# Optimization experiments

Measured on AMD Instinct MI355X. Metric: run time of the kernel, lower is better.

Reference implementation:

```python
import jax, jax.numpy as jnp
import numpy as np

BSZ, L, DIM = 2, 255, 128


def setup_inputs() -> dict:
    key = jax.random.key(0)
    k = jax.random.split(key, 8)
    d = DIM
    inv = 1.0 / np.sqrt(d)
    return {
        "x": jax.random.normal(k[0], (BSZ, L, L, d), jnp.float32),
        "mask": jax.random.randint(k[1], (BSZ, L, L), 0, 2, dtype=jnp.int32),
        "pos_embed_w": jax.random.normal(k[2], (2, d), jnp.float32) * 0.1,
        "h_qkv_w": jax.random.normal(k[3], (3 * d, d), jnp.float32) * inv,
        "h_qkv_b": jnp.zeros((3 * d,), jnp.float32),
        "v_qkv_w": jax.random.normal(k[4], (3 * d, d), jnp.float32) * inv,
        "v_qkv_b": jnp.zeros((3 * d,), jnp.float32),
        "dense_w": jax.random.normal(k[5], (d, 2 * d), jnp.float32) * (1.0 / np.sqrt(2 * d)),
        "dense_b": jnp.zeros((d,), jnp.float32),
        "ln1_g": jnp.ones((d,), jnp.float32),
        "ln1_b": jnp.zeros((d,), jnp.float32),
        "conv1_w": jax.random.normal(k[6], (d, d, 3, 3), jnp.float32) * (1.0 / np.sqrt(9 * d)),
        "conv2_w": jax.random.normal(k[7], (d, d, 3, 3), jnp.float32) * (1.0 / np.sqrt(9 * d)),
        "ln2_g": jnp.ones((d,), jnp.float32),
        "ln2_b": jnp.zeros((d,), jnp.float32),
    }


def _layer_norm(t, g, b, eps=1e-5):
    mu = t.mean(-1, keepdims=True)
    var = ((t - mu) ** 2).mean(-1, keepdims=True)
    return (t - mu) / jnp.sqrt(var + eps) * g + b


def _forward(x, mask, pos_embed_w, h_qkv_w, h_qkv_b, v_qkv_w, v_qkv_b,
             dense_w, dense_b, ln1_g, ln1_b, conv1_w, conv2_w, ln2_g, ln2_b):
    # dropout is identity (eval mode)
    bsz, L_, w, d = x.shape
    scale = np.sqrt(d)
    x = jnp.clip(x, -1000.0, 1000.0)

    # RoFormer sinusoidal table for w positions: sin/cos each (w, d//2)
    freq = 1.0 / (10000.0 ** (np.arange(0, d, 2, dtype=np.float64) / d))
    ang = np.arange(w, dtype=np.float64)[:, None] * freq[None, :]
    sin = jnp.asarray(np.sin(ang), x.dtype)
    cos = jnp.asarray(np.cos(ang), x.dtype)

    # triangular position bias: columns < w//2 get embed[0], rest embed[1]
    pos_idx = jnp.concatenate([
        jnp.zeros((w // 2,), jnp.int32), jnp.ones((w - w // 2,), jnp.int32)])
    x = x + pos_embed_w[pos_idx][None, None]  # (bsz, L, w, d)

    maskf = mask.reshape(-1, w).astype(x.dtype)            # (R, w), 1 = masked
    row_valid = mask.reshape(-1, w).sum(-1) != w            # (R,)
    add_mask = maskf[:, None, :] * -10000.0                 # (R, 1, w)

    def rotary(t):
        x1, x2 = t[..., 0::2], t[..., 1::2]
        r1 = x1 * cos - x2 * sin
        r2 = x2 * cos + x1 * sin
        return jnp.stack([r1, r2], axis=-1).reshape(t.shape)

    def attn_branch(scores, Wqkv, bqkv):
        # scores: (R, w, d)
        qkv = jnp.clip(scores @ Wqkv.T + bqkv, -10000.0, 10000.0)
        q, k, v = jnp.split(qkv, 3, axis=-1)
        q, k = rotary(q), rotary(k)
        a = jnp.clip(jnp.einsum('rqd,rkd->rqk', q, k) / scale, -10000.0, 10000.0)
        a = jax.nn.softmax(a + add_mask, axis=-1)
        a = jnp.where(maskf[:, None, :] > 0, 0.0, a)  # masked_fill after softmax
        return a @ v

    h_v = attn_branch(x.reshape(-1, w, d), h_qkv_w, h_qkv_b)

    # roll columns by (col - w//2) along rows, then flip columns
    # flipped[b,n,c] = x[b, (n - (w-1-c) + w//2) % L, w-1-c]
    cc = (w - 1) - jnp.arange(w)                                  # (w,)
    row_idx = (jnp.arange(L_)[:, None] - cc[None, :] + w // 2) % L_  # (L, w)
    v_scores = x[:, row_idx, cc[None, :]]                          # (bsz, L, w, d)
    v_v = attn_branch(v_scores.reshape(-1, w, d), v_qkv_w, v_qkv_b)

    v = jnp.concatenate([h_v, v_v], axis=-1) @ dense_w.T + dense_b
    # rows that are fully masked were never written in the torch scatter -> zero
    v = jnp.where(row_valid[:, None, None], v, 0.0)
    v = _layer_norm(v + x.reshape(-1, w, d), ln1_g, ln1_b)

    v4 = v.reshape(bsz, L_, w, d).transpose(0, 3, 1, 2)  # NCHW
    mb = mask[:, None, :, :] > 0                          # (bsz, 1, L, w)

    def mconv(t, kern):
        t = jnp.where(mb, 0.0, t)
        return jax.lax.conv_general_dilated(
            t, kern, (1, 1), 'SAME',
            dimension_numbers=('NCHW', 'OIHW', 'NCHW'))

    c = mconv(v4, conv1_w)
    c = jax.nn.gelu(c, approximate=False)
    c = mconv(c, conv2_w)
    c = c.transpose(0, 2, 3, 1).reshape(-1, w, d)
    out = _layer_norm(c + v, ln2_g, ln2_b)
    return out.reshape(bsz, L_, w, d)


def reference(x, mask, pos_embed_w, h_qkv_w, h_qkv_b, v_qkv_w, v_qkv_b,
              dense_w, dense_b, ln1_g, ln1_b, conv1_w, conv2_w, ln2_g, ln2_b):
    return _forward(x, mask, pos_embed_w, h_qkv_w, h_qkv_b, v_qkv_w, v_qkv_b,
                    dense_w, dense_b, ln1_g, ln1_b, conv1_w, conv2_w, ln2_g, ln2_b)
```

## Files before the change

### kernel.cpp

```cpp
#include <hip/hip_runtime.h>
#include <hip/hip_bf16.h>
#include <math.h>

constexpr int BSZ = 2;
constexpr int LL  = 255;
constexpr int WW  = 255;
constexpr int DD  = 128;
constexpr int RR  = BSZ * LL;
constexpr int GG  = RR * WW;

typedef __attribute__((ext_vector_type(8))) short bf16x8;
typedef __attribute__((ext_vector_type(4))) float f32x4;
typedef unsigned short ushort_t;

__device__ __forceinline__ float clip1k(float v){ return fminf(fmaxf(v, -1000.f), 1000.f); }
__device__ __forceinline__ float clipT(float v){ return fminf(fmaxf(v, -10000.f), 10000.f); }
__device__ __forceinline__ unsigned short f2bf(float f){
    unsigned int u = __float_as_uint(f);
    unsigned int r = u + 0x7fffu + ((u >> 16) & 1u);
    return (unsigned short)(r >> 16);
}
__device__ __forceinline__ float bf2f(ushort_t h){
    return __uint_as_float(((unsigned)h) << 16);
}

__global__ __launch_bounds__(64) void k_tables(const int* __restrict__ mask,
                                               float* __restrict__ sintab,
                                               float* __restrict__ costab,
                                               float* __restrict__ rv)
{
    int bid = blockIdx.x, lane = threadIdx.x;
    if (bid < RR) {
        const int* mr = mask + bid * WW;
        int s = 0;
        for (int j = lane; j < WW; j += 64) s += mr[j];
        #pragma unroll
        for (int off = 32; off > 0; off >>= 1) s += __shfl_xor(s, off);
        if (lane == 0) rv[bid] = (s != WW) ? 1.f : 0.f;
    } else {
        int base = (bid - RR) * 256;
        for (int k = 0; k < 4; k++) {
            int idx = base + k * 64 + lane;
            if (idx < WW * 64) {
                int p = idx >> 6, t = idx & 63;
                double freq = exp((double)t * (-9.210340371976184 / 64.0));
                double a = (double)p * freq;
                sintab[idx] = (float)sin(a);
                costab[idx] = (float)cos(a);
            }
        }
    }
}

__global__ __launch_bounds__(256) void k_wconv(const float* __restrict__ w1,
                                               const float* __restrict__ w2,
                                               ushort_t* __restrict__ Wt1,
                                               ushort_t* __restrict__ Wt2)
{
    int idx = blockIdx.x * 256 + threadIdx.x;
    if (idx >= 2 * 147456) return;
    int buf = idx / 147456, rem = idx % 147456;
    int o = rem / 1152, k = rem % 1152;
    int ky = k / 384, kx = (k % 384) / 128, c = k % 128;
    const float* w = buf ? w2 : w1;
    float v = w[((o * 128 + c) * 3 + ky) * 3 + kx];
    (buf ? Wt2 : Wt1)[rem] = f2bf(v);
}

__global__ __launch_bounds__(256) void k_wmisc(const float* __restrict__ hW,
                                               const float* __restrict__ vW,
                                               const float* __restrict__ dw,
                                               ushort_t* __restrict__ hWb,
                                               ushort_t* __restrict__ vWb,
                                               ushort_t* __restrict__ dwb)
{
    int idx = blockIdx.x * 256 + threadIdx.x;
    if (idx < 49152) { hWb[idx] = f2bf(hW[idx]); vWb[idx] = f2bf(vW[idx]); }
    if (idx < 32768) dwb[idx] = f2bf(dw[idx]);
}

template <int BRANCH>
__global__ __launch_bounds__(256, 2) void k_qkvm(const float* __restrict__ x,
                                                 const float* __restrict__ pe,
                                                 const ushort_t* __restrict__ Wb,
                                                 const float* __restrict__ bias,
                                                 const float* __restrict__ sintab,
                                                 const float* __restrict__ costab,
                                                 ushort_t* __restrict__ Qb,
                                                 ushort_t* __restrict__ Kb,
                                                 ushort_t* __restrict__ Vt)
{
    __shared__ ushort_t xs[128][136];
    __shared__ ushort_t os[128][136];
    const int tid = threadIdx.x;
    const int l = tid & 63, w = tid >> 6;
    const int l15 = l & 15, l4g = l >> 4;
    const int wr = w & 1, wc = w >> 1;
    const int tile0 = blockIdx.x * 128;

    for (int it = 0; it < 8; it++) {
        int idx = it * 256 + tid;
        int p = idx >> 4, c8 = idx & 15;
        int gpos = tile0 + p;
        uint4 pk = make_uint4(0u, 0u, 0u, 0u);
        if (gpos < GG) {
            int j = gpos % 255;
            const float* src;
            int pidx;
            if (BRANCH == 0) {
                src = x + (size_t)gpos * DD + c8 * 8;
                pidx = (j < 127) ? 0 : 1;
            } else {
                int b = gpos / (LL * WW);
                int rem = gpos - b * (LL * WW);
                int i = rem / WW;
                int ri = (i + j + 128) % 255;
                int cj = 254 - j;
                src = x + (size_t)((b * LL + ri) * WW + cj) * DD + c8 * 8;
                pidx = (j <= 127) ? 1 : 0;
            }
            float4 a0 = *(const float4*)src;
            float4 a1 = *(const float4*)(src + 4);
            float4 p0 = *(const float4*)(pe + pidx * DD + c8 * 8);
            float4 p1 = *(const float4*)(pe + pidx * DD + c8 * 8 + 4);
            float e0 = clip1k(a0.x) + p0.x, e1 = clip1k(a0.y) + p0.y;
            float e2 = clip1k(a0.z) + p0.z, e3 = clip1k(a0.w) + p0.w;
            float e4 = clip1k(a1.x) + p1.x, e5 = clip1k(a1.y) + p1.y;
            float e6 = clip1k(a1.z) + p1.z, e7 = clip1k(a1.w) + p1.w;
            pk.x = f2bf(e0) | ((unsigned)f2bf(e1) << 16);
            pk.y = f2bf(e2) | ((unsigned)f2bf(e3) << 16);
            pk.z = f2bf(e4) | ((unsigned)f2bf(e5) << 16);
            pk.w = f2bf(e6) | ((unsigned)f2bf(e7) << 16);
        }
        *(uint4*)(&xs[p][c8 * 8]) = pk;
    }
    __syncthreads();

    for (int part = 0; part < 3; part++) {
        f32x4 acc[4][4];
        const f32x4 z4 = {0.f, 0.f, 0.f, 0.f};
        #pragma unroll
        for (int mt = 0; mt < 4; mt++)
            #pragma unroll
            for (int nt = 0; nt < 4; nt++) acc[mt][nt] = z4;

        #pragma unroll
        for (int kk = 0; kk < 4; kk++) {
            bf16x8 af[4], bf[4];
            #pragma unroll
            for (int mt = 0; mt < 4; mt++)
                af[mt] = *(const bf16x8*)(Wb + (size_t)(part * 128 + wr * 64 + mt * 16 + l15) * 128 + kk * 32 + l4g * 8);
            #pragma unroll
            for (int nt = 0; nt < 4; nt++)
                bf[nt] = *(const bf16x8*)(&xs[wc * 64 + nt * 16 + l15][kk * 32 + l4g * 8]);
            #pragma unroll
            for (int mt = 0; mt < 4; mt++)
                #pragma unroll
                for (int nt = 0; nt < 4; nt++)
                    acc[mt][nt] = __builtin_amdgcn_mfma_f32_16x16x32_bf16(af[mt], bf[nt], acc[mt][nt], 0, 0, 0);
        }

        #pragma unroll
        for (int mt = 0; mt < 4; mt++) {
            int obase = wr * 64 + mt * 16 + l4g * 4;
            float4 bv = *(const float4*)(bias + part * 128 + obase);
            #pragma unroll
            for (int nt = 0; nt < 4; nt++) {
                int pl = wc * 64 + nt * 16 + l15;
                int gpos = tile0 + pl;
                int j = (gpos < GG) ? (gpos % 255) : 0;
                float v0 = clipT(acc[mt][nt][0] + bv.x);
                float v1 = clipT(acc[mt][nt][1] + bv.y);
                float v2 = clipT(acc[mt][nt][2] + bv.z);
                float v3 = clipT(acc[mt][nt][3] + bv.w);
                if (part < 2) {
                    int t0 = obase >> 1;
                    float cs0 = costab[j * 64 + t0],     sn0 = sintab[j * 64 + t0];
                    float cs1 = costab[j * 64 + t0 + 1], sn1 = sintab[j * 64 + t0 + 1];
                    float r0 = v0 * cs0 - v1 * sn0;
                    float r1 = v1 * cs0 + v0 * sn0;
                    float r2 = v2 * cs1 - v3 * sn1;
                    float r3 = v3 * cs1 + v2 * sn1;
                    *(unsigned*)(&os[pl][obase])     = f2bf(r0) | ((unsigned)f2bf(r1) << 16);
                    *(unsigned*)(&os[pl][obase + 2]) = f2bf(r2) | ((unsigned)f2bf(r3) << 16);
                } else {
                    os[obase + 0][pl] = f2bf(v0);
                    os[obase + 1][pl] = f2bf(v1);
                    os[obase + 2][pl] = f2bf(v2);
                    os[obase + 3][pl] = f2bf(v3);
                }
            }
        }
        __syncthreads();

        if (part < 2) {
            ushort_t* dst = (part == 0) ? Qb : Kb;
            #pragma unroll
            for (int it = 0; it < 8; it++) {
                int idx = it * 256 + tid;
                int p = idx >> 4, c8 = idx & 15;
                int gpos = tile0 + p;
                if (gpos < GG) *(uint4*)(dst + (size_t)gpos * 128 + c8 * 8) = *(const uint4*)(&os[p][c8 * 8]);
            }
        } else {
            for (int it = 0; it < 64; it++) {
                int idx = it * 256 + tid;
                int d = idx >> 7, p = idx & 127;
                int gpos = tile0 + p;
                if (gpos < GG) {
                    int rg = gpos / 255, j = gpos - rg * 255;
                    Vt[((size_t)d * 510 + rg) * 256 + j] = os[d][p];
                }
            }
        }
        __syncthreads();
    }
}

__global__ __launch_bounds__(256, 2) void k_attn2(const ushort_t* __restrict__ Qb,
                                                  const ushort_t* __restrict__ Kb,
                                                  const ushort_t* __restrict__ Vt,
                                                  const int* __restrict__ mask,
                                                  ushort_t* __restrict__ outO)
{
    __shared__ ushort_t pb[64][264];
    __shared__ float redM[64][4];
    __shared__ float redS[64][4];

    const int tid = threadIdx.x;
    const int l = tid & 63, w = tid >> 6;
    const int l15 = l & 15, l4g = l >> 4;
    const int qt = blockIdx.x, rg = blockIdx.y;
    const int q0 = qt * 64;
    const size_t rowbase = (size_t)rg * 255;
    const float iscale = 0.0883883476483184f;

    const bf16x8 zf = {0, 0, 0, 0, 0, 0, 0, 0};
    f32x4 acc[4][4];
    const f32x4 z4 = {0.f, 0.f, 0.f, 0.f};
    #pragma unroll
    for (int mt = 0; mt < 4; mt++)
        #pragma unroll
        for (int nt = 0; nt < 4; nt++) acc[mt][nt] = z4;

    #pragma unroll
    for (int kk = 0; kk < 4; kk++) {
        bf16x8 qf[4], bf[4];
        #pragma unroll
        for (int mt = 0; mt < 4; mt++) {
            int q = q0 + mt * 16 + l15;
            qf[mt] = (q < 255) ? *(const bf16x8*)(Qb + (rowbase + q) * 128 + kk * 32 + l4g * 8) : zf;
        }
        #pragma unroll
        for (int nt = 0; nt < 4; nt++) {
            int kpos = w * 64 + nt * 16 + l15;
            bf[nt] = (kpos < 255) ? *(const bf16x8*)(Kb + (rowbase + kpos) * 128 + kk * 32 + l4g * 8) : zf;
        }
        #pragma unroll
        for (int mt = 0; mt < 4; mt++)
            #pragma unroll
            for (int nt = 0; nt < 4; nt++)
                acc[mt][nt] = __builtin_amdgcn_mfma_f32_16x16x32_bf16(qf[mt], bf[nt], acc[mt][nt], 0, 0, 0);
    }

    float madd[4]; int keep[4];
    #pragma unroll
    for (int nt = 0; nt < 4; nt++) {
        int j = w * 64 + nt * 16 + l15;
        bool jv = (j < 255);
        int mv = jv ? mask[rowbase + j] : 1;
        madd[nt] = (mv > 0) ? -10000.f : 0.f;
        keep[nt] = (jv && mv == 0) ? 1 : 0;
        #pragma unroll
        for (int mt = 0; mt < 4; mt++)
            #pragma unroll
            for (int r = 0; r < 4; r++) {
                float s = jv ? (clipT(acc[mt][nt][r] * iscale) + madd[nt]) : -1e38f;
                acc[mt][nt][r] = s;
            }
    }

    float pm[4][4];
    #pragma unroll
    for (int mt = 0; mt < 4; mt++)
        #pragma unroll
        for (int r = 0; r < 4; r++) {
            float v = fmaxf(fmaxf(acc[mt][0][r], acc[mt][1][r]), fmaxf(acc[mt][2][r], acc[mt][3][r]));
            pm[mt][r] = v;
        }
    #pragma unroll
    for (int off = 1; off < 16; off <<= 1)
        #pragma unroll
        for (int mt = 0; mt < 4; mt++)
            #pragma unroll
            for (int r = 0; r < 4; r++)
                pm[mt][r] = fmaxf(pm[mt][r], __shfl_xor(pm[mt][r], off));
    if (l15 == 0) {
        #pragma unroll
        for (int mt = 0; mt < 4; mt++)
            #pragma unroll
            for (int r = 0; r < 4; r++)
                redM[mt * 16 + l4g * 4 + r][w] = pm[mt][r];
    }
    __syncthreads();
    float m[4][4];
    #pragma unroll
    for (int mt = 0; mt < 4; mt++)
        #pragma unroll
        for (int r = 0; r < 4; r++) {
            int q = mt * 16 + l4g * 4 + r;
            m[mt][r] = fmaxf(fmaxf(redM[q][0], redM[q][1]), fmaxf(redM[q][2], redM[q][3]));
        }

    float ps[4][4];
    #pragma unroll
    for (int mt = 0; mt < 4; mt++)
        #pragma unroll
        for (int r = 0; r < 4; r++) {
            float s = 0.f;
            #pragma unroll
            for (int nt = 0; nt < 4; nt++) {
                float e = __expf(acc[mt][nt][r] - m[mt][r]);
                s += e;
                acc[mt][nt][r] = keep[nt] ? e : 0.f;
            }
            ps[mt][r] = s;
        }
    #pragma unroll
    for (int off = 1; off < 16; off <<= 1)
        #pragma unroll
        for (int mt = 0; mt < 4; mt++)
            #pragma unroll
            for (int r = 0; r < 4; r++)
                ps[mt][r] += __shfl_xor(ps[mt][r], off);
    if (l15 == 0) {
        #pragma unroll
        for (int mt = 0; mt < 4; mt++)
            #pragma unroll
            for (int r = 0; r < 4; r++)
                redS[mt * 16 + l4g * 4 + r][w] = ps[mt][r];
    }
    __syncthreads();

    #pragma unroll
    for (int mt = 0; mt < 4; mt++)
        #pragma unroll
        for (int r = 0; r < 4; r++) {
            int q = mt * 16 + l4g * 4 + r;
            float inv = 1.f / (redS[q][0] + redS[q][1] + redS[q][2] + redS[q][3]);
            #pragma unroll
            for (int nt = 0; nt < 4; nt++) {
                int j = w * 64 + nt * 16 + l15;
                pb[q][j] = f2bf(acc[mt][nt][r] * inv);
            }
        }
    __syncthreads();

    f32x4 av[4][2];
    #pragma unroll
    for (int mt = 0; mt < 4; mt++) { av[mt][0] = z4; av[mt][1] = z4; }
    #pragma unroll
    for (int kk = 0; kk < 8; kk++) {
        bf16x8 pa[4], vf[2];
        #pragma unroll
        for (int mt = 0; mt < 4; mt++)
            pa[mt] = *(const bf16x8*)(&pb[mt * 16 + l15][kk * 32 + l4g * 8]);
        #pragma unroll
        for (int nt = 0; nt < 2; nt++) {
            int d = w * 32 + nt * 16 + l15;
            vf[nt] = *(const bf16x8*)(Vt + ((size_t)d * 510 + rg) * 256 + kk * 32 + l4g * 8);
        }
        #pragma unroll
        for (int mt = 0; mt < 4; mt++)
            #pragma unroll
            for (int nt = 0; nt < 2; nt++)
                av[mt][nt] = __builtin_amdgcn_mfma_f32_16x16x32_bf16(pa[mt], vf[nt], av[mt][nt], 0, 0, 0);
    }

    __syncthreads();
    ushort_t* osA = (ushort_t*)pb;
    #pragma unroll
    for (int mt = 0; mt < 4; mt++) {
        #pragma unroll
        for (int r = 0; r < 4; r++) {
            int ql = mt * 16 + l4g * 4 + r;
            #pragma unroll
            for (int nt = 0; nt < 2; nt++) {
                int d = w * 32 + nt * 16 + l15;
                osA[ql * 136 + d] = f2bf(av[mt][nt][r]);
            }
        }
    }
    __syncthreads();
    #pragma unroll
    for (int it = 0; it < 4; it++) {
        int idx = it * 256 + tid;
        int p = idx >> 4, c8 = idx & 15;
        int q = q0 + p;
        if (q < 255) *(uint4*)(outO + (rowbase + q) * 128 + c8 * 8) = *(const uint4*)(&osA[p * 136 + c8 * 8]);
    }
}

__global__ __launch_bounds__(256, 2) void k_dense2(const ushort_t* __restrict__ hv,
                                                   const ushort_t* __restrict__ vv,
                                                   const ushort_t* __restrict__ dwb,
                                                   const float* __restrict__ db,
                                                   const float* __restrict__ x,
                                                   const float* __restrict__ pe,
                                                   const float* __restrict__ rv,
                                                   const float* __restrict__ g1,
                                                   const float* __restrict__ b1,
                                                   ushort_t* __restrict__ Cb)
{
    __shared__ float redS[128][2], redQ[128][2];
    __shared__ ushort_t os[128][136];
    const int tid = threadIdx.x;
    const int l = tid & 63, w = tid >> 6;
    const int l15 = l & 15, l4g = l >> 4;
    const int wr = w & 1, wc = w >> 1;
    const int tile0 = blockIdx.x * 128;

    f32x4 acc[4][4];
    const f32x4 z4 = {0.f, 0.f, 0.f, 0.f};
    #pragma unroll
    for (int mt = 0; mt < 4; mt++)
        #pragma unroll
        for (int nt = 0; nt < 4; nt++) acc[mt][nt] = z4;

    #pragma unroll
    for (int kk = 0; kk < 8; kk++) {
        bf16x8 af[4], bf[4];
        #pragma unroll
        for (int mt = 0; mt < 4; mt++) {
            int gpos = tile0 + wr * 64 + mt * 16 + l15;
            if (gpos >= GG) gpos = GG - 1;
            const ushort_t* srcp = (kk < 4) ? (hv + (size_t)gpos * 128 + kk * 32 + l4g * 8)
                                            : (vv + (size_t)gpos * 128 + (kk - 4) * 32 + l4g * 8);
            af[mt] = *(const bf16x8*)srcp;
        }
        #pragma unroll
        for (int nt = 0; nt < 4; nt++) {
            int o = wc * 64 + nt * 16 + l15;
            bf[nt] = *(const bf16x8*)(dwb + (size_t)o * 256 + kk * 32 + l4g * 8);
        }
        #pragma unroll
        for (int mt = 0; mt < 4; mt++)
            #pragma unroll
            for (int nt = 0; nt < 4; nt++)
                acc[mt][nt] = __builtin_amdgcn_mfma_f32_16x16x32_bf16(af[mt], bf[nt], acc[mt][nt], 0, 0, 0);
    }

    #pragma unroll
    for (int mt = 0; mt < 4; mt++) {
        #pragma unroll
        for (int r = 0; r < 4; r++) {
            int row = wr * 64 + mt * 16 + l4g * 4 + r;
            int gpos = tile0 + row;
            bool valid = (gpos < GG);
            int rg = valid ? gpos / 255 : 0;
            int j = gpos - rg * 255;
            float rvv = valid ? rv[rg] : 0.f;
            int pidx = (j < 127) ? 0 : 1;
            float s1 = 0.f, s2 = 0.f;
            #pragma unroll
            for (int nt = 0; nt < 4; nt++) {
                int o = wc * 64 + nt * 16 + l15;
                float resid = 0.f;
                if (valid) resid = clip1k(x[(size_t)gpos * 128 + o]) + pe[pidx * 128 + o];
                float v = (acc[mt][nt][r] + db[o]) * rvv + resid;
                acc[mt][nt][r] = v;
                s1 += v; s2 += v * v;
            }
            s1 += __shfl_xor(s1, 1); s2 += __shfl_xor(s2, 1);
            s1 += __shfl_xor(s1, 2); s2 += __shfl_xor(s2, 2);
            s1 += __shfl_xor(s1, 4); s2 += __shfl_xor(s2, 4);
            s1 += __shfl_xor(s1, 8); s2 += __shfl_xor(s2, 8);
            if (l15 == 0) { redS[row][wc] = s1; redQ[row][wc] = s2; }
        }
    }
    __syncthreads();
    #pragma unroll
    for (int mt = 0; mt < 4; mt++) {
        #pragma unroll
        for (int r = 0; r < 4; r++) {
            int row = wr * 64 + mt * 16 + l4g * 4 + r;
            int gpos = tile0 + row;
            if (gpos >= GG) continue;
            float mu = (redS[row][0] + redS[row][1]) * 0.0078125f;
            float q  = (redQ[row][0] + redQ[row][1]) * 0.0078125f;
            float inv = rsqrtf(q - mu * mu + 1e-5f);
            #pragma unroll
            for (int nt = 0; nt < 4; nt++) {
                int o = wc * 64 + nt * 16 + l15;
                float y = (acc[mt][nt][r] - mu) * inv * g1[o] + b1[o];
                os[row][o] = f2bf(y);
            }
        }
    }
    __syncthreads();
    #pragma unroll
    for (int it = 0; it < 8; it++) {
        int idx = it * 256 + tid;
        int p = idx >> 4, c8 = idx & 15;
        int gpos = tile0 + p;
        if (gpos < GG) *(uint4*)(Cb + (size_t)gpos * 128 + c8 * 8) = *(const uint4*)(&os[p][c8 * 8]);
    }
}

template <int EPI>
__global__ __launch_bounds__(256, 2) void k_convm(const ushort_t* __restrict__ inB,
                                                  const int* __restrict__ mask,
                                                  const ushort_t* __restrict__ Wt,
                                                  const ushort_t* __restrict__ vbB,
                                                  const float* __restrict__ g2,
                                                  const float* __restrict__ b2,
                                                  ushort_t* __restrict__ outB,
                                                  float* __restrict__ outF)
{
    __shared__ ushort_t s_a[132][136];
    __shared__ ushort_t s_b[2][128][40];
    __shared__ float redS[128][2], redQ[128][2];

    const int tid = threadIdx.x;
    const int l  = tid & 63, lrn = l & 15, lgp = l >> 4;
    const int w  = tid >> 6, wr = w & 1, wc = w >> 1;
    const int r  = blockIdx.y, b = r / LL, i = r % LL;
    const int j0 = blockIdx.x * 128;

    f32x4 acc[4][4];
    const f32x4 z4 = {0.f, 0.f, 0.f, 0.f};
    #pragma unroll
    for (int jt = 0; jt < 4; jt++)
        #pragma unroll
        for (int ot = 0; ot < 4; ot++) acc[jt][ot] = z4;

    for (int ky = 0; ky < 3; ky++) {
        const int ri = i + ky - 1;
        for (int t = tid; t < 132 * 16; t += 256) {
            int col = t >> 4, c8 = t & 15;
            int nj = j0 - 1 + col;
            int4 pk = make_int4(0, 0, 0, 0);
            if (ri >= 0 && ri < LL && nj >= 0 && nj < WW) {
                int mp = (b * LL + ri) * WW + nj;
                if (mask[mp] == 0) pk = *(const int4*)(inB + (size_t)mp * DD + c8 * 8);
            }
            *(int4*)(&s_a[col][c8 * 8]) = pk;
        }
        {
            const int kb = ky * 384;
            #pragma unroll
            for (int it = 0; it < 2; it++) {
                int idx = it * 256 + tid, o = idx >> 2, q = idx & 3;
                *(int4*)(&s_b[0][o][q * 8]) = *(const int4*)(Wt + (size_t)o * 1152 + kb + q * 8);
            }
        }
        __syncthreads();

        for (int s = 0; s < 12; s++) {
            if (s < 11) {
                const int kb = ky * 384 + (s + 1) * 32;
                const int bufn = (s + 1) & 1;
                #pragma unroll
                for (int it = 0; it < 2; it++) {
                    int idx = it * 256 + tid, o = idx >> 2, q = idx & 3;
                    *(int4*)(&s_b[bufn][o][q * 8]) = *(const int4*)(Wt + (size_t)o * 1152 + kb + q * 8);
                }
            }
            const int kx = s >> 2;
            const int c0 = (s & 3) * 32 + lgp * 8;
            const int buf = s & 1;
            bf16x8 af[4], bfr[4];
            #pragma unroll
            for (int jt = 0; jt < 4; jt++) {
                int col = wr * 64 + jt * 16 + lrn + kx;
                af[jt] = *(const bf16x8*)(&s_a[col][c0]);
            }
            #pragma unroll
            for (int ot = 0; ot < 4; ot++) {
                int o = wc * 64 + ot * 16 + lrn;
                bfr[ot] = *(const bf16x8*)(&s_b[buf][o][lgp * 8]);
            }
            #pragma unroll
            for (int jt = 0; jt < 4; jt++)
                #pragma unroll
                for (int ot = 0; ot < 4; ot++)
                    acc[jt][ot] = __builtin_amdgcn_mfma_f32_16x16x32_bf16(af[jt], bfr[ot], acc[jt][ot], 0, 0, 0);
            __syncthreads();
        }
    }

    if (EPI == 0) {
        #pragma unroll
        for (int jt = 0; jt < 4; jt++) {
            #pragma unroll
            for (int r4 = 0; r4 < 4; r4++) {
                int jl = wr * 64 + jt * 16 + lgp * 4 + r4;
                #pragma unroll
                for (int ot = 0; ot < 4; ot++) {
                    int o = wc * 64 + ot * 16 + lrn;
                    float a = acc[jt][ot][r4];
                    float y = 0.5f * a * (1.f + erff(a * 0.70710678118654752f));
                    s_a[jl][o] = f2bf(y);
                }
            }
        }
        __syncthreads();
        #pragma unroll
        for (int it = 0; it < 8; it++) {
            int idx = it * 256 + tid;
            int p = idx >> 4, c8 = idx & 15;
            int j = j0 + p;
            if (j < WW) {
                size_t gp = (size_t)((b * LL + i) * WW + j) * DD;
                *(uint4*)(outB + gp + c8 * 8) = *(const uint4*)(&s_a[p][c8 * 8]);
            }
        }
    } else {
        #pragma unroll
        for (int it = 0; it < 8; it++) {
            int idx = it * 256 + tid;
            int p = idx >> 4, c8 = idx & 15;
            int j = j0 + p;
            uint4 v = make_uint4(0u, 0u, 0u, 0u);
            if (j < WW) v = *(const uint4*)(vbB + (size_t)((b * LL + i) * WW + j) * DD + c8 * 8);
            *(uint4*)(&s_a[p][c8 * 8]) = v;
        }
        __syncthreads();

        float g2v[4], b2v[4];
        #pragma unroll
        for (int ot = 0; ot < 4; ot++) {
            int o = wc * 64 + ot * 16 + lrn;
            g2v[ot] = g2[o]; b2v[ot] = b2[o];
        }
        #pragma unroll
        for (int jt = 0; jt < 4; jt++) {
            #pragma unroll
            for (int r4 = 0; r4 < 4; r4++) {
                int jl = wr * 64 + jt * 16 + lgp * 4 + r4;
                int j = j0 + jl;
                float s1 = 0.f, s2 = 0.f;
                if (j < WW) {
                    #pragma unroll
                    for (int ot = 0; ot < 4; ot++) {
                        int o = wc * 64 + ot * 16 + lrn;
                        float v = acc[jt][ot][r4] + bf2f(s_a[jl][o]);
                        acc[jt][ot][r4] = v;
                        s1 += v; s2 += v * v;
                    }
                }
                #pragma unroll
                for (int off = 1; off < 16; off <<= 1) {
                    s1 += __shfl_xor(s1, off);
                    s2 += __shfl_xor(s2, off);
                }
                if (lrn == 0) { redS[jl][wc] = s1; redQ[jl][wc] = s2; }
            }
        }
        __syncthreads();
        #pragma unroll
        for (int jt = 0; jt < 4; jt++) {
            #pragma unroll
            for (int r4 = 0; r4 < 4; r4++) {
                int jl = wr * 64 + jt * 16 + lgp * 4 + r4;
                int j = j0 + jl;
                if (j >= WW) continue;
                float mu = (redS[jl][0] + redS[jl][1]) * 0.0078125f;
                float q  = (redQ[jl][0] + redQ[jl][1]) * 0.0078125f;
                float inv = rsqrtf(q - mu * mu + 1e-5f);
                size_t gp = (size_t)((b * LL + i) * WW + j) * DD;
                #pragma unroll
                for (int ot = 0; ot < 4; ot++) {
                    int o = wc * 64 + ot * 16 + lrn;
                    outF[gp + o] = (acc[jt][ot][r4] - mu) * inv * g2v[ot] + b2v[ot];
                }
            }
        }
    }
}

extern "C" void kernel_launch(void* const* d_in, const int* in_sizes, int n_in,
                              void* d_out, int out_size, void* d_ws, size_t ws_size,
                              hipStream_t stream)
{
    (void)in_sizes; (void)n_in; (void)out_size; (void)ws_size;
    const float* x    = (const float*)d_in[0];
    const int*   mask = (const int*)d_in[1];
    const float* pe   = (const float*)d_in[2];
    const float* hW   = (const float*)d_in[3];
    const float* hb   = (const float*)d_in[4];
    const float* vW   = (const float*)d_in[5];
    const float* vbias= (const float*)d_in[6];
    const float* dw   = (const float*)d_in[7];
    const float* db   = (const float*)d_in[8];
    const float* g1   = (const float*)d_in[9];
    const float* b1   = (const float*)d_in[10];
    const float* w1   = (const float*)d_in[11];
    const float* w2   = (const float*)d_in[12];
    const float* g2   = (const float*)d_in[13];
    const float* b2   = (const float*)d_in[14];
    float* out = (float*)d_out;

    char* ws = (char*)d_ws;
    float* sintab = (float*)(ws + 0);
    float* costab = (float*)(ws + 65536);
    float* rvbuf  = (float*)(ws + 131072);
    ushort_t* hWb = (ushort_t*)(ws + 143360);
    ushort_t* vWb = (ushort_t*)(ws + 241664);
    ushort_t* dwb = (ushort_t*)(ws + 339968);
    ushort_t* Wt1 = (ushort_t*)(ws + 405504);
    ushort_t* Wt2 = (ushort_t*)(ws + 700416);

    const size_t R0 = 2097152;
    ushort_t* Qb = (ushort_t*)(ws + R0);
    ushort_t* Kb = (ushort_t*)(ws + R0 + 33292800);
    ushort_t* Vt = (ushort_t*)(ws + R0 + 66585600);
    ushort_t* Cb = (ushort_t*)(ws + R0 + 66585600);
    ushort_t* hvb = (ushort_t*)(ws + 102760448);
    ushort_t* vvb = (ushort_t*)(ws + 136314880);
    ushort_t* c1b = vvb;

    k_tables<<<RR + 64, 64, 0, stream>>>(mask, sintab, costab, rvbuf);
    k_wconv<<<1152, 256, 0, stream>>>(w1, w2, Wt1, Wt2);
    k_wmisc<<<192, 256, 0, stream>>>(hW, vW, dw, hWb, vWb, dwb);

    k_qkvm<0><<<1017, 256, 0, stream>>>(x, pe, hWb, hb, sintab, costab, Qb, Kb, Vt);
    k_attn2<<<dim3(4, RR), 256, 0, stream>>>(Qb, Kb, Vt, mask, hvb);
    k_qkvm<1><<<1017, 256, 0, stream>>>(x, pe, vWb, vbias, sintab, costab, Qb, Kb, Vt);
    k_attn2<<<dim3(4, RR), 256, 0, stream>>>(Qb, Kb, Vt, mask, vvb);

    k_dense2<<<1017, 256, 0, stream>>>(hvb, vvb, dwb, db, x, pe, rvbuf, g1, b1, Cb);
    k_convm<0><<<dim3(2, RR), 256, 0, stream>>>(Cb, mask, Wt1, nullptr, nullptr, nullptr, c1b, nullptr);
    k_convm<1><<<dim3(2, RR), 256, 0, stream>>>(c1b, mask, Wt2, Cb, g2, b2, nullptr, out);
}
```

Baseline: 566.2 us.

## Cut LDS use and raise occupancy across qkv, dense and conv kernels

```diff
diff --git a/kernel.cpp b/kernel.cpp
--- a/kernel.cpp
+++ b/kernel.cpp
@@ -64,7 +64,10 @@
     int ky = k / 384, kx = (k % 384) / 128, c = k % 128;
     const float* w = buf ? w2 : w1;
     float v = w[((o * 128 + c) * 3 + ky) * 3 + kx];
-    (buf ? Wt2 : Wt1)[rem] = f2bf(v);
+    int s_sub = kx * 4 + (c >> 5);
+    int lgp = (c >> 3) & 3, e = c & 7;
+    int flat = (((ky * 12 + s_sub) * 128 + o) * 4 + lgp) * 8 + e;
+    (buf ? Wt2 : Wt1)[flat] = f2bf(v);
 }
 
 __global__ __launch_bounds__(256) void k_wmisc(const float* __restrict__ hW,
@@ -80,7 +83,7 @@
 }
 
 template <int BRANCH>
-__global__ __launch_bounds__(256, 2) void k_qkvm(const float* __restrict__ x,
+__global__ __launch_bounds__(256, 3) void k_qkvm(const float* __restrict__ x,
                                                  const float* __restrict__ pe,
                                                  const ushort_t* __restrict__ Wb,
                                                  const float* __restrict__ bias,
@@ -91,7 +94,7 @@
                                                  ushort_t* __restrict__ Vt)
 {
     __shared__ ushort_t xs[128][136];
-    __shared__ ushort_t os[128][136];
+    __shared__ ushort_t os2[8192];
     const int tid = threadIdx.x;
     const int l = tid & 63, w = tid >> 6;
     const int l15 = l & 15, l4g = l >> 4;
@@ -160,64 +163,73 @@
                     acc[mt][nt] = __builtin_amdgcn_mfma_f32_16x16x32_bf16(af[mt], bf[nt], acc[mt][nt], 0, 0, 0);
         }
 
-        #pragma unroll
-        for (int mt = 0; mt < 4; mt++) {
-            int obase = wr * 64 + mt * 16 + l4g * 4;
-            float4 bv = *(const float4*)(bias + part * 128 + obase);
-            #pragma unroll
-            for (int nt = 0; nt < 4; nt++) {
-                int pl = wc * 64 + nt * 16 + l15;
-                int gpos = tile0 + pl;
-                int j = (gpos < GG) ? (gpos % 255) : 0;
-                float v0 = clipT(acc[mt][nt][0] + bv.x);
-                float v1 = clipT(acc[mt][nt][1] + bv.y);
-                float v2 = clipT(acc[mt][nt][2] + bv.z);
-                float v3 = clipT(acc[mt][nt][3] + bv.w);
-                if (part < 2) {
-                    int t0 = obase >> 1;
-                    float cs0 = costab[j * 64 + t0],     sn0 = sintab[j * 64 + t0];
-                    float cs1 = costab[j * 64 + t0 + 1], sn1 = sintab[j * 64 + t0 + 1];
-                    float r0 = v0 * cs0 - v1 * sn0;
-                    float r1 = v1 * cs0 + v0 * sn0;
-                    float r2 = v2 * cs1 - v3 * sn1;
-                    float r3 = v3 * cs1 + v2 * sn1;
-                    *(unsigned*)(&os[pl][obase])     = f2bf(r0) | ((unsigned)f2bf(r1) << 16);
-                    *(unsigned*)(&os[pl][obase + 2]) = f2bf(r2) | ((unsigned)f2bf(r3) << 16);
-                } else {
-                    os[obase + 0][pl] = f2bf(v0);
-                    os[obase + 1][pl] = f2bf(v1);
-                    os[obase + 2][pl] = f2bf(v2);
-                    os[obase + 3][pl] = f2bf(v3);
+        for (int h = 0; h < 2; h++) {
+            if (wr == h) {
+                #pragma unroll
+                for (int mt = 0; mt < 4; mt++) {
+                    int obase = h * 64 + mt * 16 + l4g * 4;
+                    float4 bv = *(const float4*)(bias + part * 128 + obase);
+                    #pragma unroll
+                    for (int nt = 0; nt < 4; nt++) {
+                        int pl = wc * 64 + nt * 16 + l15;
+                        int gpos = tile0 + pl;
+                        int j = (gpos < GG) ? (gpos % 255) : 0;
+                        float v0 = clipT(acc[mt][nt][0] + bv.x);
+                        float v1 = clipT(acc[mt][nt][1] + bv.y);
+                        float v2 = clipT(acc[mt][nt][2] + bv.z);
+                        float v3 = clipT(acc[mt][nt][3] + bv.w);
+                        if (part < 2) {
+                            int t0 = obase >> 1;
+                            float cs0 = costab[j * 64 + t0],     sn0 = sintab[j * 64 + t0];
+                            float cs1 = costab[j * 64 + t0 + 1], sn1 = sintab[j * 64 + t0 + 1];
+                            float r0 = v0 * cs0 - v1 * sn0;
+                            float r1 = v1 * cs0 + v0 * sn0;
+                            float r2 = v2 * cs1 - v3 * sn1;
+                            float r3 = v3 * cs1 + v2 * sn1;
+                            int cb = mt * 16 + l4g * 4;
+                            int sx = (cb >> 3) ^ (pl & 7);
+                            int base = pl * 64 + sx * 8 + (cb & 7);
+                            *(unsigned*)(&os2[base])     = f2bf(r0) | ((unsigned)f2bf(r1) << 16);
+                            *(unsigned*)(&os2[base + 2]) = f2bf(r2) | ((unsigned)f2bf(r3) << 16);
+                        } else {
+                            int d0 = mt * 16 + l4g * 4;
+                            os2[(d0 + 0) * 128 + pl] = f2bf(v0);
+                            os2[(d0 + 1) * 128 + pl] = f2bf(v1);
+                            os2[(d0 + 2) * 128 + pl] = f2bf(v2);
+                            os2[(d0 + 3) * 128 + pl] = f2bf(v3);
+                        }
+                    }
                 }
             }
-        }
-        __syncthreads();
-
-        if (part < 2) {
-            ushort_t* dst = (part == 0) ? Qb : Kb;
-            #pragma unroll
-            for (int it = 0; it < 8; it++) {
-                int idx = it * 256 + tid;
-                int p = idx >> 4, c8 = idx & 15;
-                int gpos = tile0 + p;
-                if (gpos < GG) *(uint4*)(dst + (size_t)gpos * 128 + c8 * 8) = *(const uint4*)(&os[p][c8 * 8]);
-            }
-        } else {
-            for (int it = 0; it < 64; it++) {
-                int idx = it * 256 + tid;
-                int d = idx >> 7, p = idx & 127;
-                int gpos = tile0 + p;
-                if (gpos < GG) {
-                    int rg = gpos / 255, j = gpos - rg * 255;
-                    Vt[((size_t)d * 510 + rg) * 256 + j] = os[d][p];
+            __syncthreads();
+            if (part < 2) {
+                ushort_t* dst = (part == 0) ? Qb : Kb;
+                #pragma unroll
+                for (int it = 0; it < 4; it++) {
+                    int idx = it * 256 + tid;
+                    int p = idx >> 3, c8 = idx & 7;
+                    int gpos = tile0 + p;
+                    int sx = c8 ^ (p & 7);
+                    if (gpos < GG)
+                        *(uint4*)(dst + (size_t)gpos * 128 + h * 64 + c8 * 8) = *(const uint4*)(&os2[p * 64 + sx * 8]);
                 }
-            }
-        }
-        __syncthreads();
-    }
-}
-
-__global__ __launch_bounds__(256, 2) void k_attn2(const ushort_t* __restrict__ Qb,
+            } else {
+                for (int it = 0; it < 32; it++) {
+                    int idx = it * 256 + tid;
+                    int d = idx >> 7, p = idx & 127;
+                    int gpos = tile0 + p;
+                    if (gpos < GG) {
+                        int rg = gpos / 255, j = gpos - rg * 255;
+                        Vt[((size_t)(h * 64 + d) * 510 + rg) * 256 + j] = os2[d * 128 + p];
+                    }
+                }
+            }
+            __syncthreads();
+        }
+    }
+}
+
+__global__ __launch_bounds__(256, 4) void k_attn2(const ushort_t* __restrict__ Qb,
                                                   const ushort_t* __restrict__ Kb,
                                                   const ushort_t* __restrict__ Vt,
                                                   const int* __restrict__ mask,
@@ -401,7 +413,7 @@
     }
 }
 
-__global__ __launch_bounds__(256, 2) void k_dense2(const ushort_t* __restrict__ hv,
+__global__ __launch_bounds__(256, 4) void k_dense2(const ushort_t* __restrict__ hv,
                                                    const ushort_t* __restrict__ vv,
                                                    const ushort_t* __restrict__ dwb,
                                                    const float* __restrict__ db,
@@ -420,6 +432,31 @@
     const int wr = w & 1, wc = w >> 1;
     const int tile0 = blockIdx.x * 128;
 
+    for (int it = 0; it < 8; it++) {
+        int idx = it * 256 + tid;
+        int p = idx >> 4, c8 = idx & 15;
+        int gpos = tile0 + p;
+        uint4 pk = make_uint4(0u, 0u, 0u, 0u);
+        if (gpos < GG) {
+            int j = gpos % 255;
+            int pidx = (j < 127) ? 0 : 1;
+            const float* src = x + (size_t)gpos * DD + c8 * 8;
+            float4 a0 = *(const float4*)src;
+            float4 a1 = *(const float4*)(src + 4);
+            float4 p0 = *(const float4*)(pe + pidx * DD + c8 * 8);
+            float4 p1 = *(const float4*)(pe + pidx * DD + c8 * 8 + 4);
+            float e0 = clip1k(a0.x) + p0.x, e1 = clip1k(a0.y) + p0.y;
+            float e2 = clip1k(a0.z) + p0.z, e3 = clip1k(a0.w) + p0.w;
+            float e4 = clip1k(a1.x) + p1.x, e5 = clip1k(a1.y) + p1.y;
+            float e6 = clip1k(a1.z) + p1.z, e7 = clip1k(a1.w) + p1.w;
+            pk.x = f2bf(e0) | ((unsigned)f2bf(e1) << 16);
+            pk.y = f2bf(e2) | ((unsigned)f2bf(e3) << 16);
+            pk.z = f2bf(e4) | ((unsigned)f2bf(e5) << 16);
+            pk.w = f2bf(e6) | ((unsigned)f2bf(e7) << 16);
+        }
+        *(uint4*)(&os[p][c8 * 8]) = pk;
+    }
+
     f32x4 acc[4][4];
     const f32x4 z4 = {0.f, 0.f, 0.f, 0.f};
     #pragma unroll
@@ -449,6 +486,7 @@
             for (int nt = 0; nt < 4; nt++)
                 acc[mt][nt] = __builtin_amdgcn_mfma_f32_16x16x32_bf16(af[mt], bf[nt], acc[mt][nt], 0, 0, 0);
     }
+    __syncthreads();
 
     #pragma unroll
     for (int mt = 0; mt < 4; mt++) {
@@ -458,15 +496,12 @@
             int gpos = tile0 + row;
             bool valid = (gpos < GG);
             int rg = valid ? gpos / 255 : 0;
-            int j = gpos - rg * 255;
             float rvv = valid ? rv[rg] : 0.f;
-            int pidx = (j < 127) ? 0 : 1;
             float s1 = 0.f, s2 = 0.f;
             #pragma unroll
             for (int nt = 0; nt < 4; nt++) {
                 int o = wc * 64 + nt * 16 + l15;
-                float resid = 0.f;
-                if (valid) resid = clip1k(x[(size_t)gpos * 128 + o]) + pe[pidx * 128 + o];
+                float resid = bf2f(os[row][o]);
                 float v = (acc[mt][nt][r] + db[o]) * rvv + resid;
                 acc[mt][nt][r] = v;
                 s1 += v; s2 += v * v;
@@ -508,7 +543,7 @@
 }
 
 template <int EPI>
-__global__ __launch_bounds__(256, 2) void k_convm(const ushort_t* __restrict__ inB,
+__global__ __launch_bounds__(256, 4) void k_convm(const ushort_t* __restrict__ inB,
                                                   const int* __restrict__ mask,
                                                   const ushort_t* __restrict__ Wt,
                                                   const ushort_t* __restrict__ vbB,
@@ -518,7 +553,6 @@
                                                   float* __restrict__ outF)
 {
     __shared__ ushort_t s_a[132][136];
-    __shared__ ushort_t s_b[2][128][40];
     __shared__ float redS[128][2], redQ[128][2];
 
     const int tid = threadIdx.x;
@@ -546,29 +580,11 @@
             }
             *(int4*)(&s_a[col][c8 * 8]) = pk;
         }
-        {
-            const int kb = ky * 384;
-            #pragma unroll
-            for (int it = 0; it < 2; it++) {
-                int idx = it * 256 + tid, o = idx >> 2, q = idx & 3;
-                *(int4*)(&s_b[0][o][q * 8]) = *(const int4*)(Wt + (size_t)o * 1152 + kb + q * 8);
-            }
-        }
         __syncthreads();
 
         for (int s = 0; s < 12; s++) {
-            if (s < 11) {
-                const int kb = ky * 384 + (s + 1) * 32;
-                const int bufn = (s + 1) & 1;
-                #pragma unroll
-                for (int it = 0; it < 2; it++) {
-                    int idx = it * 256 + tid, o = idx >> 2, q = idx & 3;
-                    *(int4*)(&s_b[bufn][o][q * 8]) = *(const int4*)(Wt + (size_t)o * 1152 + kb + q * 8);
-                }
-            }
             const int kx = s >> 2;
             const int c0 = (s & 3) * 32 + lgp * 8;
-            const int buf = s & 1;
             bf16x8 af[4], bfr[4];
             #pragma unroll
             for (int jt = 0; jt < 4; jt++) {
@@ -578,15 +594,15 @@
             #pragma unroll
             for (int ot = 0; ot < 4; ot++) {
                 int o = wc * 64 + ot * 16 + lrn;
-                bfr[ot] = *(const bf16x8*)(&s_b[buf][o][lgp * 8]);
+                bfr[ot] = *(const bf16x8*)(Wt + ((size_t)((ky * 12 + s) * 128 + o) * 4 + lgp) * 8);
             }
             #pragma unroll
             for (int jt = 0; jt < 4; jt++)
                 #pragma unroll
                 for (int ot = 0; ot < 4; ot++)
                     acc[jt][ot] = __builtin_amdgcn_mfma_f32_16x16x32_bf16(af[jt], bfr[ot], acc[jt][ot], 0, 0, 0);
-            __syncthreads();
-        }
+        }
+        __syncthreads();
     }
 
     if (EPI == 0) {
```

Result: slower. 852.8 us (+50.6%).
